# Kernel optimization log

Hardware: AMD Instinct MI355X
Metric: run time of the kernel (lower is better)

Reference implementation:

```python
import jax, jax.numpy as jnp
import numpy as np

N_NODES = 100000
N_EDGES = 3200000
N_GRAPHS = 4096
IN_DIM = 128
HID = 64
EPS = 1e-5


def setup_inputs() -> dict:
    key = jax.random.key(0)
    ks = jax.random.split(key, 16)
    x = jax.random.normal(ks[0], (N_NODES, IN_DIM), dtype=jnp.float32)
    edge_index = jax.random.randint(ks[1], (2, N_EDGES), 0, N_NODES, dtype=jnp.int32)
    batch = jnp.sort(jax.random.randint(ks[2], (N_NODES,), 0, N_GRAPHS, dtype=jnp.int32))

    def lin(k, fan_in, fan_out):
        s = 1.0 / np.sqrt(fan_in)
        kw, kb = jax.random.split(k)
        W = jax.random.uniform(kw, (fan_in, fan_out), minval=-s, maxval=s, dtype=jnp.float32)
        b = jax.random.uniform(kb, (fan_out,), minval=-s, maxval=s, dtype=jnp.float32)
        return W, b

    Wc0, bc0 = lin(ks[3], IN_DIM, HID)
    Wc1, bc1 = lin(ks[4], HID, HID)
    Wc2, bc2 = lin(ks[5], HID, HID)
    W1, b1 = lin(ks[6], HID, HID)
    W2, b2 = lin(ks[7], HID, 1)
    ones = jnp.ones((HID,), jnp.float32)
    zeros = jnp.zeros((HID,), jnp.float32)
    return {
        'x': x, 'edge_index': edge_index, 'batch': batch,
        'Wc0': Wc0, 'bc0': bc0, 'g0': ones, 'be0': zeros,
        'Wc1': Wc1, 'bc1': bc1, 'g1': ones, 'be1': zeros,
        'Wc2': Wc2, 'bc2': bc2, 'g2': ones, 'be2': zeros,
        'W1': W1, 'b1': b1, 'gf': ones, 'bf': zeros,
        'W2': W2, 'b2': b2,
    }


def _gcn_norm(edge_index):
    # Add self-loops, then symmetric normalization norm_e = d^-1/2[row] * d^-1/2[col]
    loops = jnp.arange(N_NODES, dtype=jnp.int32)
    row = jnp.concatenate([edge_index[0], loops])
    col = jnp.concatenate([edge_index[1], loops])
    deg = jax.ops.segment_sum(jnp.ones_like(col, jnp.float32), col, num_segments=N_NODES)
    dinv = jnp.where(deg > 0, jax.lax.rsqrt(deg), 0.0)
    norm = dinv[row] * dinv[col]
    return row, col, norm


def _gcn_conv(x, W, b, row, col, norm):
    h = x @ W                                   # [N, hid]
    msg = h[row] * norm[:, None]                # [E+N, hid] gather + scale
    out = jax.ops.segment_sum(msg, col, num_segments=N_NODES)  # scatter-add
    return out + b


def _bn(x, gamma, beta):
    mu = jnp.mean(x, axis=0)
    var = jnp.var(x, axis=0)
    return (x - mu) * jax.lax.rsqrt(var + EPS) * gamma + beta


def reference(x, edge_index, batch, Wc0, bc0, g0, be0, Wc1, bc1, g1, be1,
              Wc2, bc2, g2, be2, W1, b1, gf, bf, W2, b2):
    row, col, norm = _gcn_norm(edge_index)
    h = x
    for W, b, g, be in ((Wc0, bc0, g0, be0), (Wc1, bc1, g1, be1), (Wc2, bc2, g2, be2)):
        h = jax.nn.relu(_bn(_gcn_conv(h, W, b, row, col, norm), g, be))
    # global mean pool over graphs
    sums = jax.ops.segment_sum(h, batch, num_segments=N_GRAPHS)
    cnts = jax.ops.segment_sum(jnp.ones((N_NODES,), jnp.float32), batch, num_segments=N_GRAPHS)
    pooled = sums / jnp.maximum(cnts, 1.0)[:, None]  # [G, hid]
    z = jax.nn.relu(_bn(pooled @ W1 + b1, gf, bf))
    # dropout is identity at inference
    out = z @ W2 + b2
    return out.squeeze(-1)
```

## Files before the change

kernel.cpp:

```cpp
#include <hip/hip_runtime.h>
#include <hip/hip_bf16.h>

#define NN 100000
#define NE 3200000
#define NG 4096
#define NB 128
#define NBK 782

typedef unsigned short ushort_t;

__device__ __forceinline__ float bf2f(unsigned short u){
  union{unsigned int i; float f;} x; x.i = ((unsigned)u)<<16; return x.f;
}
__device__ __forceinline__ ushort_t f2bf(float f){
  union{float f; unsigned int i;} x; x.f = f;
  unsigned int r = x.i + 0x7fff + ((x.i >> 16) & 1);
  return (ushort_t)(r >> 16);
}


__global__ __launch_bounds__(256) void k_hist(const int* __restrict__ ei, int* __restrict__ histT){
  __shared__ int lh[NBK];
  int b = blockIdx.x, t = threadIdx.x;
  for (int k=t; k<NBK; k+=256) lh[k]=0;
  __syncthreads();
  int e0 = b*(NE/NB);
  for (int e=e0+t; e<e0+(NE/NB); e+=256) atomicAdd(&lh[ei[NE+e]>>7], 1);
  __syncthreads();
  for (int k=t; k<NBK; k+=256) histT[k*NB+b] = lh[k];
}

__global__ __launch_bounds__(256) void k_scanA(int* __restrict__ histT, int* __restrict__ total){
  int wv = blockIdx.x*4 + (threadIdx.x>>6);
  int lane = threadIdx.x & 63;
  if (wv >= NBK) return;
  int* row = histT + wv*NB;
  int a0 = row[lane], a1 = row[64+lane];
  int i0 = a0, i1 = a1;
  for (int off=1; off<64; off<<=1){
    int x = __shfl_up(i0, off, 64);
    int y = __shfl_up(i1, off, 64);
    if (lane >= off){ i0 += x; i1 += y; }
  }
  i1 += __shfl(i0, 63, 64);
  row[lane]    = i0 - a0;
  row[64+lane] = i1 - a1;
  if (lane==63) total[wv] = i1;
}

__global__ void k_scanB(const int* __restrict__ total, int* __restrict__ base){
  __shared__ int lds[1024];
  int t = threadIdx.x;
  int v = (t < NBK)? total[t] : 0;
  lds[t] = v; __syncthreads();
  for (int off=1; off<1024; off<<=1){
    int x = (t>=off)? lds[t-off] : 0;
    __syncthreads();
    lds[t] += x;
    __syncthreads();
  }
  if (t < NBK)      base[t]   = lds[t]-v;
  if (t == NBK-1)   base[NBK] = lds[t];
}

__global__ __launch_bounds__(256) void k_pairs(const int* __restrict__ ei,
    const int* __restrict__ histT, const int* __restrict__ base,
    int* __restrict__ pairs){
  __shared__ int cur[NBK];
  int b = blockIdx.x, t = threadIdx.x;
  for (int k=t; k<NBK; k+=256) cur[k] = base[k] + histT[k*NB + b];
  __syncthreads();
  int e0 = b*(NE/NB);
  for (int e=e0+t; e<e0+(NE/NB); e+=256){
    int src = ei[e], dst = ei[NE+e];
    int p = atomicAdd(&cur[dst>>7], 1);
    pairs[p] = (src << 7) | (dst & 127);
  }
}

__global__ __launch_bounds__(256) void k_fine(const int* __restrict__ pairs,
    const int* __restrict__ base, int* __restrict__ csr,
    int* __restrict__ colptr, float* __restrict__ dinv){
  __shared__ int cnt[128], off[128];
  int k = blockIdx.x, t = threadIdx.x;
  if (t < 128) cnt[t] = 0;
  __syncthreads();
  int s = base[k], e = base[k+1];
  for (int i=s+t; i<e; i+=256) atomicAdd(&cnt[pairs[i] & 127], 1);
  __syncthreads();
  int v = (t<128)? cnt[t] : 0;
  if (t<128) off[t] = v;
  __syncthreads();
  for (int o=1; o<128; o<<=1){
    int x = (t>=o && t<128)? off[t-o] : 0;
    __syncthreads();
    if (t<128) off[t] += x;
    __syncthreads();
  }
  int node0 = k*128;
  if (t < 128 && node0+t < NN){
    colptr[node0+t] = s + off[t] - v;
    dinv[node0+t]   = rsqrtf((float)cnt[t] + 1.0f);
  }
  if (k == NBK-1 && t == 0) colptr[NN] = NE;
  __syncthreads();
  if (t < 128) cnt[t] = off[t] - v;
  __syncthreads();
  for (int i=s+t; i<e; i+=256){
    int u = pairs[i];
    int p = s + atomicAdd(&cnt[u & 127], 1);
    csr[p] = u >> 7;
  }
}


template<int K>
__global__ __launch_bounds__(256) void k_gemm(const float* __restrict__ in_,
    const float* __restrict__ W, const float* __restrict__ dinv,
    ushort_t* __restrict__ out){
  __shared__ float Wl[K*64];
  int t = threadIdx.x;
  for (int i=t; i<K*64; i+=256) Wl[i] = W[i];
  __syncthreads();
  int c  = t & 63;
  int vb = __builtin_amdgcn_readfirstlane((int)(blockIdx.x*16 + (t>>6)*4));
  float acc0=0.f, acc1=0.f, acc2=0.f, acc3=0.f;
  const float4* x0 = (const float4*)(in_ + (size_t)vb*K);
  constexpr int RS = K/4;
  #pragma unroll 4
  for (int k4=0;k4<K/4;++k4){
    float4 a0 = x0[k4], a1 = x0[k4+RS], a2 = x0[k4+2*RS], a3 = x0[k4+3*RS];
    const float* wr = &Wl[k4*4*64 + c];
    float w0=wr[0], w1=wr[64], w2=wr[128], w3=wr[192];
    acc0 = fmaf(a0.x,w0,fmaf(a0.y,w1,fmaf(a0.z,w2,fmaf(a0.w,w3,acc0))));
    acc1 = fmaf(a1.x,w0,fmaf(a1.y,w1,fmaf(a1.z,w2,fmaf(a1.w,w3,acc1))));
    acc2 = fmaf(a2.x,w0,fmaf(a2.y,w1,fmaf(a2.z,w2,fmaf(a2.w,w3,acc2))));
    acc3 = fmaf(a3.x,w0,fmaf(a3.y,w1,fmaf(a3.z,w2,fmaf(a3.w,w3,acc3))));
  }
  float d0=dinv[vb], d1=dinv[vb+1], d2=dinv[vb+2], d3=dinv[vb+3];
  out[(size_t)(vb+0)*64+c]=f2bf(acc0*d0);
  out[(size_t)(vb+1)*64+c]=f2bf(acc1*d1);
  out[(size_t)(vb+2)*64+c]=f2bf(acc2*d2);
  out[(size_t)(vb+3)*64+c]=f2bf(acc3*d3);
}


__global__ __launch_bounds__(256) void k_aggregate(const ushort_t* __restrict__ hs,
    const int* __restrict__ colptr, const int* __restrict__ csr,
    const float* __restrict__ dinv, const float* __restrict__ bias,
    float* __restrict__ out, float* __restrict__ stats){
  int t = threadIdx.x; int c = t & 63;
  int wv = blockIdx.x*4 + (t>>6);
  float bc = bias[c];
  float s1 = 0.f, s2 = 0.f;
  for (int v = wv; v < NN; v += 8192){
    int vv = __builtin_amdgcn_readfirstlane(v);
    int e0 = colptr[vv], e1 = colptr[vv+1];
    float acc = bf2f(hs[(size_t)vv*64 + c]);
    int e = e0;
    for (; e+4 <= e1; e += 4){
      int i0=csr[e], i1=csr[e+1], i2=csr[e+2], i3=csr[e+3];
      float f0=bf2f(hs[(size_t)i0*64+c]), f1=bf2f(hs[(size_t)i1*64+c]);
      float f2=bf2f(hs[(size_t)i2*64+c]), f3=bf2f(hs[(size_t)i3*64+c]);
      acc += (f0+f1)+(f2+f3);
    }
    for (; e<e1; ++e) acc += bf2f(hs[(size_t)csr[e]*64+c]);
    float o = acc*dinv[vv] + bc;
    out[(size_t)vv*64+c] = o;
    s1 += o; s2 += o*o;
  }
  __shared__ float l1[256], l2[256];
  l1[t]=s1; l2[t]=s2; __syncthreads();
  if (t < 64){
    float a1 = l1[t]+l1[t+64]+l1[t+128]+l1[t+192];
    float a2 = l2[t]+l2[t+64]+l2[t+128]+l2[t+192];
    float* rep = stats + (size_t)(blockIdx.x & 31)*128;
    atomicAdd(&rep[t],    a1);
    atomicAdd(&rep[64+t], a2);
  }
}


__global__ void k_bncoeff(const float* __restrict__ stats, const float* __restrict__ g,
                          const float* __restrict__ be, float cnt, float* __restrict__ coeff){
  int c = threadIdx.x;
  float s1=0.f, s2=0.f;
  for (int r=0;r<32;++r){ s1 += stats[r*128+c]; s2 += stats[r*128+64+c]; }
  float mu  = s1/cnt;
  float var = s2/cnt - mu*mu;
  float a   = g[c]*rsqrtf(var + 1e-5f);
  coeff[c]    = a;
  coeff[64+c] = be[c] - mu*a;
}

__global__ __launch_bounds__(256) void k_bnapply(float* __restrict__ buf, const float* __restrict__ cf){
  int i = blockIdx.x*256 + threadIdx.x;
  float4 v = ((float4*)buf)[i];
  int c0 = (i & 15)*4;
  float a0=cf[c0+0], a1=cf[c0+1], a2=cf[c0+2], a3=cf[c0+3];
  float d0=cf[64+c0+0], d1=cf[64+c0+1], d2=cf[64+c0+2], d3=cf[64+c0+3];
  v.x = fmaxf(fmaf(v.x,a0,d0),0.f);
  v.y = fmaxf(fmaf(v.y,a1,d1),0.f);
  v.z = fmaxf(fmaf(v.z,a2,d2),0.f);
  v.w = fmaxf(fmaf(v.w,a3,d3),0.f);
  ((float4*)buf)[i] = v;
}


__global__ __launch_bounds__(256) void k_gbounds(const int* __restrict__ batch, int* __restrict__ gstart){
  int g = blockIdx.x*256 + threadIdx.x;
  int lo=0, hi=NN;
  while (lo<hi){ int mid=(lo+hi)>>1; if (batch[mid]<g) lo=mid+1; else hi=mid; }
  gstart[g]=lo;
  if (g==0) gstart[NG]=NN;
}

__global__ __launch_bounds__(256) void k_pool(const float* __restrict__ h, const int* __restrict__ gstart,
                                              float* __restrict__ pooled){
  int t=threadIdx.x; int c=t&63;
  int g = __builtin_amdgcn_readfirstlane((int)(blockIdx.x*4 + (t>>6)));
  int s = gstart[g], e = gstart[g+1];
  float acc=0.f;
  for (int v=s; v<e; ++v) acc += h[(size_t)v*64+c];
  float inv = 1.0f / fmaxf((float)(e-s), 1.0f);
  pooled[(size_t)g*64+c] = acc*inv;
}

__global__ __launch_bounds__(256) void k_tkern(float* __restrict__ pooled, const float* __restrict__ W1,
                                               const float* __restrict__ b1, float* __restrict__ stats){
  int t=threadIdx.x; int c=t&63;
  int g = __builtin_amdgcn_readfirstlane((int)(blockIdx.x*4 + (t>>6)));
  const float* p = pooled + (size_t)g*64;
  float acc = b1[c];
  #pragma unroll 4
  for (int k=0;k<64;++k) acc = fmaf(p[k], W1[k*64+c], acc);
  pooled[(size_t)g*64+c] = acc;
  float* rep = stats + (size_t)(blockIdx.x & 31)*128;
  atomicAdd(&rep[c],    acc);
  atomicAdd(&rep[64+c], acc*acc);
}

__global__ __launch_bounds__(256) void k_final(const float* __restrict__ tbuf, const float* __restrict__ gcf,
                                               const float* __restrict__ W2, const float* __restrict__ b2,
                                               float* __restrict__ out){
  int t=threadIdx.x; int c=t&63;
  int g = blockIdx.x*4 + (t>>6);
  float tv = tbuf[(size_t)g*64+c];
  float z  = fmaxf(fmaf(tv, gcf[c], gcf[64+c]), 0.f);
  float p  = z * W2[c];
  #pragma unroll
  for (int o=32;o>0;o>>=1) p += __shfl_xor(p, o, 64);
  if (c==0) out[g] = p + b2[0];
}


extern "C" void kernel_launch(void* const* d_in, const int* in_sizes, int n_in,
                              void* d_out, int out_size, void* d_ws, size_t ws_size,
                              hipStream_t stream) {
  const float* x    = (const float*)d_in[0];
  const int*   ei   = (const int*)d_in[1];
  const int*   batch= (const int*)d_in[2];
  const float* Wc0=(const float*)d_in[3],  *bc0=(const float*)d_in[4];
  const float* g0 =(const float*)d_in[5],  *be0=(const float*)d_in[6];
  const float* Wc1=(const float*)d_in[7],  *bc1=(const float*)d_in[8];
  const float* g1 =(const float*)d_in[9],  *be1=(const float*)d_in[10];
  const float* Wc2=(const float*)d_in[11], *bc2=(const float*)d_in[12];
  const float* g2 =(const float*)d_in[13], *be2=(const float*)d_in[14];
  const float* W1 =(const float*)d_in[15], *b1 =(const float*)d_in[16];
  const float* gf =(const float*)d_in[17], *bf_=(const float*)d_in[18];
  const float* W2 =(const float*)d_in[19], *b2 =(const float*)d_in[20];
  float* out = (float*)d_out;

  char* w = (char*)d_ws;
  float*    stats  = (float*)   (w + 0);
  int*      histT  = (int*)     (w + 65536);
  int*      total  = (int*)     (w + 465920);
  int*      base   = (int*)     (w + 469056);
  int*      colptr = (int*)     (w + 472192);
  float*    dinv   = (float*)   (w + 872208);
  int*      gstart = (int*)     (w + 1272208);
  float*    coeff  = (float*)   (w + 1288608);
  float*    gcoeff = (float*)   (w + 1289120);
  float*    pooled = (float*)   (w + 1289632);
  int*      csr    = (int*)     (w + 2338240);
  ushort_t* bufA   = (ushort_t*)(w + 15138240);
  float*    bufB   = (float*)   (w + 27938240);
  int*      pairs  = (int*)bufB;

  hipMemsetAsync(stats, 0, 65536, stream);

  k_hist <<<NB,  256,  0, stream>>>(ei, histT);
  k_scanA<<<196, 256,  0, stream>>>(histT, total);
  k_scanB<<<1,   1024, 0, stream>>>(total, base);
  k_pairs<<<NB,  256,  0, stream>>>(ei, histT, base, pairs);
  k_fine <<<NBK, 256,  0, stream>>>(pairs, base, csr, colptr, dinv);

  k_gemm<128><<<NN/16, 256, 0, stream>>>(x, Wc0, dinv, bufA);
  k_aggregate<<<2048, 256, 0, stream>>>(bufA, colptr, csr, dinv, bc0, bufB, stats + 0*4096);
  k_bncoeff<<<1, 64, 0, stream>>>(stats + 0*4096, g0, be0, (float)NN, coeff);
  k_bnapply<<<NN*16/256, 256, 0, stream>>>(bufB, coeff);
  k_gemm<64><<<NN/16, 256, 0, stream>>>(bufB, Wc1, dinv, bufA);
  k_aggregate<<<2048, 256, 0, stream>>>(bufA, colptr, csr, dinv, bc1, bufB, stats + 1*4096);
  k_bncoeff<<<1, 64, 0, stream>>>(stats + 1*4096, g1, be1, (float)NN, coeff);
  k_bnapply<<<NN*16/256, 256, 0, stream>>>(bufB, coeff);
  k_gemm<64><<<NN/16, 256, 0, stream>>>(bufB, Wc2, dinv, bufA);
  k_aggregate<<<2048, 256, 0, stream>>>(bufA, colptr, csr, dinv, bc2, bufB, stats + 2*4096);
  k_bncoeff<<<1, 64, 0, stream>>>(stats + 2*4096, g2, be2, (float)NN, coeff);
  k_bnapply<<<NN*16/256, 256, 0, stream>>>(bufB, coeff);

  k_gbounds<<<NG/256, 256, 0, stream>>>(batch, gstart);
  k_pool   <<<NG/4,   256, 0, stream>>>(bufB, gstart, pooled);
  k_tkern  <<<NG/4,   256, 0, stream>>>(pooled, W1, b1, stats + 3*4096);
  k_bncoeff<<<1, 64, 0, stream>>>(stats + 3*4096, gf, bf_, (float)NG, gcoeff);
  k_final  <<<NG/4,   256, 0, stream>>>(pooled, gcoeff, W2, b2, out);
}
```

Measured before the change: 674.2 us.

## Split feature matrices into 16-column strips and aggregate one strip per pass

The bf16 node features and the fp32 layer outputs are stored as four 16-column strips instead of one 64-wide row. Aggregation now runs four passes, each gathering only one strip, so the gathered working set per pass (about 3.2 MB) is more likely to stay in cache, at the cost of reading the CSR indices four times and making four times as many launches. The GEMM, bnapply and pool kernels are adapted to the strip layout. The CSR build also doubles its block count and block size, and histT now reuses the csr buffer's space.

```diff
diff --git a/kernel.cpp b/kernel.cpp
--- a/kernel.cpp
+++ b/kernel.cpp
@@ -4,8 +4,9 @@
 #define NN 100000
 #define NE 3200000
 #define NG 4096
-#define NB 128
+#define NB 256
 #define NBK 782
+#define NST 4
 
 typedef unsigned short ushort_t;
 
@@ -19,33 +20,35 @@
 }
 
 
-__global__ __launch_bounds__(256) void k_hist(const int* __restrict__ ei, int* __restrict__ histT){
+__global__ __launch_bounds__(512) void k_hist(const int* __restrict__ ei, int* __restrict__ histT){
   __shared__ int lh[NBK];
   int b = blockIdx.x, t = threadIdx.x;
-  for (int k=t; k<NBK; k+=256) lh[k]=0;
+  for (int k=t; k<NBK; k+=512) lh[k]=0;
   __syncthreads();
   int e0 = b*(NE/NB);
-  for (int e=e0+t; e<e0+(NE/NB); e+=256) atomicAdd(&lh[ei[NE+e]>>7], 1);
-  __syncthreads();
-  for (int k=t; k<NBK; k+=256) histT[k*NB+b] = lh[k];
+  for (int e=e0+t; e<e0+(NE/NB); e+=512) atomicAdd(&lh[ei[NE+e]>>7], 1);
+  __syncthreads();
+  for (int k=t; k<NBK; k+=512) histT[(size_t)k*NB+b] = lh[k];
 }
 
 __global__ __launch_bounds__(256) void k_scanA(int* __restrict__ histT, int* __restrict__ total){
   int wv = blockIdx.x*4 + (threadIdx.x>>6);
   int lane = threadIdx.x & 63;
   if (wv >= NBK) return;
-  int* row = histT + wv*NB;
-  int a0 = row[lane], a1 = row[64+lane];
-  int i0 = a0, i1 = a1;
-  for (int off=1; off<64; off<<=1){
-    int x = __shfl_up(i0, off, 64);
-    int y = __shfl_up(i1, off, 64);
-    if (lane >= off){ i0 += x; i1 += y; }
-  }
-  i1 += __shfl(i0, 63, 64);
-  row[lane]    = i0 - a0;
-  row[64+lane] = i1 - a1;
-  if (lane==63) total[wv] = i1;
+  int* row = histT + (size_t)wv*NB;
+  int carry = 0;
+  #pragma unroll
+  for (int ch=0; ch<NB/64; ++ch){
+    int a = row[ch*64+lane];
+    int inc = a;
+    for (int off=1; off<64; off<<=1){
+      int x = __shfl_up(inc, off, 64);
+      if (lane >= off) inc += x;
+    }
+    row[ch*64+lane] = carry + inc - a;
+    carry += __shfl(inc, 63, 64);
+  }
+  if (lane==0) total[wv] = carry;
 }
 
 __global__ void k_scanB(const int* __restrict__ total, int* __restrict__ base){
@@ -63,15 +66,15 @@
   if (t == NBK-1)   base[NBK] = lds[t];
 }
 
-__global__ __launch_bounds__(256) void k_pairs(const int* __restrict__ ei,
+__global__ __launch_bounds__(512) void k_pairs(const int* __restrict__ ei,
     const int* __restrict__ histT, const int* __restrict__ base,
     int* __restrict__ pairs){
   __shared__ int cur[NBK];
   int b = blockIdx.x, t = threadIdx.x;
-  for (int k=t; k<NBK; k+=256) cur[k] = base[k] + histT[k*NB + b];
+  for (int k=t; k<NBK; k+=512) cur[k] = base[k] + histT[(size_t)k*NB + b];
   __syncthreads();
   int e0 = b*(NE/NB);
-  for (int e=e0+t; e<e0+(NE/NB); e+=256){
+  for (int e=e0+t; e<e0+(NE/NB); e+=512){
     int src = ei[e], dst = ei[NE+e];
     int p = atomicAdd(&cur[dst>>7], 1);
     pairs[p] = (src << 7) | (dst & 127);
@@ -114,22 +117,20 @@
 }
 
 
-template<int K>
-__global__ __launch_bounds__(256) void k_gemm(const float* __restrict__ in_,
+__global__ __launch_bounds__(256) void k_gemm0(const float* __restrict__ in_,
     const float* __restrict__ W, const float* __restrict__ dinv,
     ushort_t* __restrict__ out){
-  __shared__ float Wl[K*64];
+  __shared__ float Wl[128*64];
   int t = threadIdx.x;
-  for (int i=t; i<K*64; i+=256) Wl[i] = W[i];
+  for (int i=t; i<128*64; i+=256) Wl[i] = W[i];
   __syncthreads();
   int c  = t & 63;
   int vb = __builtin_amdgcn_readfirstlane((int)(blockIdx.x*16 + (t>>6)*4));
   float acc0=0.f, acc1=0.f, acc2=0.f, acc3=0.f;
-  const float4* x0 = (const float4*)(in_ + (size_t)vb*K);
-  constexpr int RS = K/4;
+  const float4* x0 = (const float4*)(in_ + (size_t)vb*128);
   #pragma unroll 4
-  for (int k4=0;k4<K/4;++k4){
-    float4 a0 = x0[k4], a1 = x0[k4+RS], a2 = x0[k4+2*RS], a3 = x0[k4+3*RS];
+  for (int k4=0;k4<32;++k4){
+    float4 a0 = x0[k4], a1 = x0[k4+32], a2 = x0[k4+64], a3 = x0[k4+96];
     const float* wr = &Wl[k4*4*64 + c];
     float w0=wr[0], w1=wr[64], w2=wr[128], w3=wr[192];
     acc0 = fmaf(a0.x,w0,fmaf(a0.y,w1,fmaf(a0.z,w2,fmaf(a0.w,w3,acc0))));
@@ -138,45 +139,83 @@
     acc3 = fmaf(a3.x,w0,fmaf(a3.y,w1,fmaf(a3.z,w2,fmaf(a3.w,w3,acc3))));
   }
   float d0=dinv[vb], d1=dinv[vb+1], d2=dinv[vb+2], d3=dinv[vb+3];
-  out[(size_t)(vb+0)*64+c]=f2bf(acc0*d0);
-  out[(size_t)(vb+1)*64+c]=f2bf(acc1*d1);
-  out[(size_t)(vb+2)*64+c]=f2bf(acc2*d2);
-  out[(size_t)(vb+3)*64+c]=f2bf(acc3*d3);
-}
-
-
-__global__ __launch_bounds__(256) void k_aggregate(const ushort_t* __restrict__ hs,
+  size_t sb = (size_t)(c>>4)*NN*16 + (c&15);
+  out[sb + (size_t)(vb+0)*16]=f2bf(acc0*d0);
+  out[sb + (size_t)(vb+1)*16]=f2bf(acc1*d1);
+  out[sb + (size_t)(vb+2)*16]=f2bf(acc2*d2);
+  out[sb + (size_t)(vb+3)*16]=f2bf(acc3*d3);
+}
+
+
+__global__ __launch_bounds__(256) void k_gemmS(const float* __restrict__ in_,
+    const float* __restrict__ W, const float* __restrict__ dinv,
+    ushort_t* __restrict__ out){
+  __shared__ float Wl[64*64];
+  int t = threadIdx.x;
+  for (int i=t; i<64*64; i+=256) Wl[i] = W[i];
+  __syncthreads();
+  int c  = t & 63;
+  int vb = __builtin_amdgcn_readfirstlane((int)(blockIdx.x*16 + (t>>6)*4));
+  float acc0=0.f, acc1=0.f, acc2=0.f, acc3=0.f;
+  #pragma unroll
+  for (int s=0;s<4;++s){
+    const float4* xs0 = (const float4*)(in_ + ((size_t)s*NN + vb+0)*16);
+    const float4* xs1 = (const float4*)(in_ + ((size_t)s*NN + vb+1)*16);
+    const float4* xs2 = (const float4*)(in_ + ((size_t)s*NN + vb+2)*16);
+    const float4* xs3 = (const float4*)(in_ + ((size_t)s*NN + vb+3)*16);
+    #pragma unroll
+    for (int j=0;j<4;++j){
+      float4 a0 = xs0[j], a1 = xs1[j], a2 = xs2[j], a3 = xs3[j];
+      const float* wr = &Wl[(s*16 + j*4)*64 + c];
+      float w0=wr[0], w1=wr[64], w2=wr[128], w3=wr[192];
+      acc0 = fmaf(a0.x,w0,fmaf(a0.y,w1,fmaf(a0.z,w2,fmaf(a0.w,w3,acc0))));
+      acc1 = fmaf(a1.x,w0,fmaf(a1.y,w1,fmaf(a1.z,w2,fmaf(a1.w,w3,acc1))));
+      acc2 = fmaf(a2.x,w0,fmaf(a2.y,w1,fmaf(a2.z,w2,fmaf(a2.w,w3,acc2))));
+      acc3 = fmaf(a3.x,w0,fmaf(a3.y,w1,fmaf(a3.z,w2,fmaf(a3.w,w3,acc3))));
+    }
+  }
+  float d0=dinv[vb], d1=dinv[vb+1], d2=dinv[vb+2], d3=dinv[vb+3];
+  size_t sb = (size_t)(c>>4)*NN*16 + (c&15);
+  out[sb + (size_t)(vb+0)*16]=f2bf(acc0*d0);
+  out[sb + (size_t)(vb+1)*16]=f2bf(acc1*d1);
+  out[sb + (size_t)(vb+2)*16]=f2bf(acc2*d2);
+  out[sb + (size_t)(vb+3)*16]=f2bf(acc3*d3);
+}
+
+
+__global__ __launch_bounds__(256) void k_aggstrip(const ushort_t* __restrict__ hsS,
     const int* __restrict__ colptr, const int* __restrict__ csr,
     const float* __restrict__ dinv, const float* __restrict__ bias,
-    float* __restrict__ out, float* __restrict__ stats){
-  int t = threadIdx.x; int c = t & 63;
-  int wv = blockIdx.x*4 + (t>>6);
-  float bc = bias[c];
-  float s1 = 0.f, s2 = 0.f;
-  for (int v = wv; v < NN; v += 8192){
-    int vv = __builtin_amdgcn_readfirstlane(v);
-    int e0 = colptr[vv], e1 = colptr[vv+1];
-    float acc = bf2f(hs[(size_t)vv*64 + c]);
-    int e = e0;
-    for (; e+4 <= e1; e += 4){
-      int i0=csr[e], i1=csr[e+1], i2=csr[e+2], i3=csr[e+3];
-      float f0=bf2f(hs[(size_t)i0*64+c]), f1=bf2f(hs[(size_t)i1*64+c]);
-      float f2=bf2f(hs[(size_t)i2*64+c]), f3=bf2f(hs[(size_t)i3*64+c]);
-      acc += (f0+f1)+(f2+f3);
-    }
-    for (; e<e1; ++e) acc += bf2f(hs[(size_t)csr[e]*64+c]);
-    float o = acc*dinv[vv] + bc;
-    out[(size_t)vv*64+c] = o;
-    s1 += o; s2 += o*o;
-  }
+    float* __restrict__ outS, float* __restrict__ stats, int s){
+  int t = threadIdx.x;
+  int cc = t & 15;
+  int grp = t >> 4;
+  int vv = blockIdx.x*16 + grp;
+  const ushort_t* strip = hsS + (size_t)s*NN*16;
+  int e0 = colptr[vv], e1 = colptr[vv+1];
+  float acc = bf2f(strip[(size_t)vv*16+cc]);
+  int e = e0;
+  for (; e < e1 && (e & 3); ++e) acc += bf2f(strip[(size_t)csr[e]*16+cc]);
+  for (; e+4 <= e1; e += 4){
+    int4 q = *(const int4*)(csr + e);
+    float f0 = bf2f(strip[(size_t)q.x*16+cc]);
+    float f1 = bf2f(strip[(size_t)q.y*16+cc]);
+    float f2 = bf2f(strip[(size_t)q.z*16+cc]);
+    float f3 = bf2f(strip[(size_t)q.w*16+cc]);
+    acc += (f0+f1)+(f2+f3);
+  }
+  for (; e<e1; ++e) acc += bf2f(strip[(size_t)csr[e]*16+cc]);
+  float o = acc*dinv[vv] + bias[s*16+cc];
+  outS[((size_t)s*NN + vv)*16 + cc] = o;
   __shared__ float l1[256], l2[256];
-  l1[t]=s1; l2[t]=s2; __syncthreads();
-  if (t < 64){
-    float a1 = l1[t]+l1[t+64]+l1[t+128]+l1[t+192];
-    float a2 = l2[t]+l2[t+64]+l2[t+128]+l2[t+192];
+  l1[t]=o; l2[t]=o*o; __syncthreads();
+  if (t < 16){
+    float a1=0.f, a2=0.f;
+    #pragma unroll
+    for (int g=0; g<16; ++g){ a1 += l1[g*16+t]; a2 += l2[g*16+t]; }
     float* rep = stats + (size_t)(blockIdx.x & 31)*128;
-    atomicAdd(&rep[t],    a1);
-    atomicAdd(&rep[64+t], a2);
+    atomicAdd(&rep[s*16+t],      a1);
+    atomicAdd(&rep[64+s*16+t],   a2);
   }
 }
 
@@ -195,8 +234,9 @@
 
 __global__ __launch_bounds__(256) void k_bnapply(float* __restrict__ buf, const float* __restrict__ cf){
   int i = blockIdx.x*256 + threadIdx.x;
-  float4 v = ((float4*)buf)[i];
-  int c0 = (i & 15)*4;
+  float4 v = ((const float4*)buf)[i];
+  int s  = i / (NN*4);
+  int c0 = s*16 + (i & 3)*4;
   float a0=cf[c0+0], a1=cf[c0+1], a2=cf[c0+2], a3=cf[c0+3];
   float d0=cf[64+c0+0], d1=cf[64+c0+1], d2=cf[64+c0+2], d3=cf[64+c0+3];
   v.x = fmaxf(fmaf(v.x,a0,d0),0.f);
@@ -220,8 +260,9 @@
   int t=threadIdx.x; int c=t&63;
   int g = __builtin_amdgcn_readfirstlane((int)(blockIdx.x*4 + (t>>6)));
   int s = gstart[g], e = gstart[g+1];
+  const float* hp = h + (size_t)(c>>4)*NN*16 + (c&15);
   float acc=0.f;
-  for (int v=s; v<e; ++v) acc += h[(size_t)v*64+c];
+  for (int v=s; v<e; ++v) acc += hp[(size_t)v*16];
   float inv = 1.0f / fmaxf((float)(e-s), 1.0f);
   pooled[(size_t)g*64+c] = acc*inv;
 }
@@ -273,38 +314,41 @@
 
   char* w = (char*)d_ws;
   float*    stats  = (float*)   (w + 0);
-  int*      histT  = (int*)     (w + 65536);
-  int*      total  = (int*)     (w + 465920);
-  int*      base   = (int*)     (w + 469056);
-  int*      colptr = (int*)     (w + 472192);
-  float*    dinv   = (float*)   (w + 872208);
-  int*      gstart = (int*)     (w + 1272208);
-  float*    coeff  = (float*)   (w + 1288608);
-  float*    gcoeff = (float*)   (w + 1289120);
-  float*    pooled = (float*)   (w + 1289632);
-  int*      csr    = (int*)     (w + 2338240);
-  ushort_t* bufA   = (ushort_t*)(w + 15138240);
-  float*    bufB   = (float*)   (w + 27938240);
+  int*      total  = (int*)     (w + 65536);
+  int*      base   = (int*)     (w + 68736);
+  int*      colptr = (int*)     (w + 71936);
+  float*    dinv   = (float*)   (w + 471952);
+  int*      gstart = (int*)     (w + 871952);
+  float*    coeff  = (float*)   (w + 888352);
+  float*    gcoeff = (float*)   (w + 888864);
+  float*    pooled = (float*)   (w + 889392);
+  int*      csr    = (int*)     (w + 1937968);
+  ushort_t* bufA   = (ushort_t*)(w + 14737968);
+  float*    bufB   = (float*)   (w + 27537968);
+  int*      histT  = csr;
   int*      pairs  = (int*)bufB;
 
   hipMemsetAsync(stats, 0, 65536, stream);
 
-  k_hist <<<NB,  256,  0, stream>>>(ei, histT);
+  k_hist <<<NB,  512,  0, stream>>>(ei, histT);
   k_scanA<<<196, 256,  0, stream>>>(histT, total);
   k_scanB<<<1,   1024, 0, stream>>>(total, base);
-  k_pairs<<<NB,  256,  0, stream>>>(ei, histT, base, pairs);
+  k_pairs<<<NB,  512,  0, stream>>>(ei, histT, base, pairs);
   k_fine <<<NBK, 256,  0, stream>>>(pairs, base, csr, colptr, dinv);
 
-  k_gemm<128><<<NN/16, 256, 0, stream>>>(x, Wc0, dinv, bufA);
-  k_aggregate<<<2048, 256, 0, stream>>>(bufA, colptr, csr, dinv, bc0, bufB, stats + 0*4096);
+  k_gemm0<<<NN/16, 256, 0, stream>>>(x, Wc0, dinv, bufA);
+  for (int s=0;s<NST;++s)
+    k_aggstrip<<<NN/16, 256, 0, stream>>>(bufA, colptr, csr, dinv, bc0, bufB, stats + 0*4096, s);
   k_bncoeff<<<1, 64, 0, stream>>>(stats + 0*4096, g0, be0, (float)NN, coeff);
   k_bnapply<<<NN*16/256, 256, 0, stream>>>(bufB, coeff);
-  k_gemm<64><<<NN/16, 256, 0, stream>>>(bufB, Wc1, dinv, bufA);
-  k_aggregate<<<2048, 256, 0, stream>>>(bufA, colptr, csr, dinv, bc1, bufB, stats + 1*4096);
+  k_gemmS<<<NN/16, 256, 0, stream>>>(bufB, Wc1, dinv, bufA);
+  for (int s=0;s<NST;++s)
+    k_aggstrip<<<NN/16, 256, 0, stream>>>(bufA, colptr, csr, dinv, bc1, bufB, stats + 1*4096, s);
   k_bncoeff<<<1, 64, 0, stream>>>(stats + 1*4096, g1, be1, (float)NN, coeff);
   k_bnapply<<<NN*16/256, 256, 0, stream>>>(bufB, coeff);
-  k_gemm<64><<<NN/16, 256, 0, stream>>>(bufB, Wc2, dinv, bufA);
-  k_aggregate<<<2048, 256, 0, stream>>>(bufA, colptr, csr, dinv, bc2, bufB, stats + 2*4096);
+  k_gemmS<<<NN/16, 256, 0, stream>>>(bufB, Wc2, dinv, bufA);
+  for (int s=0;s<NST;++s)
+    k_aggstrip<<<NN/16, 256, 0, stream>>>(bufA, colptr, csr, dinv, bc2, bufB, stats + 2*4096, s);
   k_bncoeff<<<1, 64, 0, stream>>>(stats + 2*4096, g2, be2, (float)NN, coeff);
   k_bnapply<<<NN*16/256, 256, 0, stream>>>(bufB, coeff);
 
```

Result: slower. 856.2 us (+27.0%).

## Partition CSR neighbors by source range and aggregate in phased source-range passes

Applied to the files above, without the earlier changes.

The CSR build now sorts each destination's neighbors into four source-index ranges and records per-range sub-pointers. The aggregation kernel keeps 25 node accumulators per thread and processes one source range at a time across all its nodes, with a block barrier between phases. The goal is to confine gathers from the bf16 feature buffer to a quarter-sized working set so they hit in cache more often. The histogram and pair kernels also move to 256 blocks of 512 threads, and workspace buffers are reordered and aliased. In exchange it adds register pressure, a larger sub-pointer array and barrier stalls, and less parallelism per node.

```diff
diff --git a/kernel.cpp b/kernel.cpp
--- a/kernel.cpp
+++ b/kernel.cpp
@@ -4,8 +4,9 @@
 #define NN 100000
 #define NE 3200000
 #define NG 4096
-#define NB 128
+#define NB 256
 #define NBK 782
+#define RSZ 25000
 
 typedef unsigned short ushort_t;
 
@@ -17,35 +18,40 @@
   unsigned int r = x.i + 0x7fff + ((x.i >> 16) & 1);
   return (ushort_t)(r >> 16);
 }
-
-
-__global__ __launch_bounds__(256) void k_hist(const int* __restrict__ ei, int* __restrict__ histT){
+__device__ __forceinline__ int src_rng(int s){
+  return (s>=RSZ) + (s>=2*RSZ) + (s>=3*RSZ);
+}
+
+
+__global__ __launch_bounds__(512) void k_hist(const int* __restrict__ ei, int* __restrict__ histT){
   __shared__ int lh[NBK];
   int b = blockIdx.x, t = threadIdx.x;
-  for (int k=t; k<NBK; k+=256) lh[k]=0;
+  for (int k=t; k<NBK; k+=512) lh[k]=0;
   __syncthreads();
   int e0 = b*(NE/NB);
-  for (int e=e0+t; e<e0+(NE/NB); e+=256) atomicAdd(&lh[ei[NE+e]>>7], 1);
-  __syncthreads();
-  for (int k=t; k<NBK; k+=256) histT[k*NB+b] = lh[k];
+  for (int e=e0+t; e<e0+(NE/NB); e+=512) atomicAdd(&lh[ei[NE+e]>>7], 1);
+  __syncthreads();
+  for (int k=t; k<NBK; k+=512) histT[(size_t)k*NB+b] = lh[k];
 }
 
 __global__ __launch_bounds__(256) void k_scanA(int* __restrict__ histT, int* __restrict__ total){
   int wv = blockIdx.x*4 + (threadIdx.x>>6);
   int lane = threadIdx.x & 63;
   if (wv >= NBK) return;
-  int* row = histT + wv*NB;
-  int a0 = row[lane], a1 = row[64+lane];
-  int i0 = a0, i1 = a1;
-  for (int off=1; off<64; off<<=1){
-    int x = __shfl_up(i0, off, 64);
-    int y = __shfl_up(i1, off, 64);
-    if (lane >= off){ i0 += x; i1 += y; }
-  }
-  i1 += __shfl(i0, 63, 64);
-  row[lane]    = i0 - a0;
-  row[64+lane] = i1 - a1;
-  if (lane==63) total[wv] = i1;
+  int* row = histT + (size_t)wv*NB;
+  int carry = 0;
+  #pragma unroll
+  for (int ch=0; ch<NB/64; ++ch){
+    int a = row[ch*64+lane];
+    int inc = a;
+    for (int off=1; off<64; off<<=1){
+      int x = __shfl_up(inc, off, 64);
+      if (lane >= off) inc += x;
+    }
+    row[ch*64+lane] = carry + inc - a;
+    carry += __shfl(inc, 63, 64);
+  }
+  if (lane==0) total[wv] = carry;
 }
 
 __global__ void k_scanB(const int* __restrict__ total, int* __restrict__ base){
@@ -63,15 +69,15 @@
   if (t == NBK-1)   base[NBK] = lds[t];
 }
 
-__global__ __launch_bounds__(256) void k_pairs(const int* __restrict__ ei,
+__global__ __launch_bounds__(512) void k_pairs(const int* __restrict__ ei,
     const int* __restrict__ histT, const int* __restrict__ base,
     int* __restrict__ pairs){
   __shared__ int cur[NBK];
   int b = blockIdx.x, t = threadIdx.x;
-  for (int k=t; k<NBK; k+=256) cur[k] = base[k] + histT[k*NB + b];
+  for (int k=t; k<NBK; k+=512) cur[k] = base[k] + histT[(size_t)k*NB + b];
   __syncthreads();
   int e0 = b*(NE/NB);
-  for (int e=e0+t; e<e0+(NE/NB); e+=256){
+  for (int e=e0+t; e<e0+(NE/NB); e+=512){
     int src = ei[e], dst = ei[NE+e];
     int p = atomicAdd(&cur[dst>>7], 1);
     pairs[p] = (src << 7) | (dst & 127);
@@ -80,36 +86,50 @@
 
 __global__ __launch_bounds__(256) void k_fine(const int* __restrict__ pairs,
     const int* __restrict__ base, int* __restrict__ csr,
-    int* __restrict__ colptr, float* __restrict__ dinv){
-  __shared__ int cnt[128], off[128];
+    int* __restrict__ colptr, int* __restrict__ subp, float* __restrict__ dinv){
+  __shared__ int cnt[512], off[512], ps[256];
   int k = blockIdx.x, t = threadIdx.x;
-  if (t < 128) cnt[t] = 0;
+  cnt[t]=0; cnt[t+256]=0;
   __syncthreads();
   int s = base[k], e = base[k+1];
-  for (int i=s+t; i<e; i+=256) atomicAdd(&cnt[pairs[i] & 127], 1);
-  __syncthreads();
-  int v = (t<128)? cnt[t] : 0;
-  if (t<128) off[t] = v;
-  __syncthreads();
-  for (int o=1; o<128; o<<=1){
-    int x = (t>=o && t<128)? off[t-o] : 0;
-    __syncthreads();
-    if (t<128) off[t] += x;
-    __syncthreads();
-  }
+  for (int i=s+t; i<e; i+=256){
+    int u = pairs[i];
+    atomicAdd(&cnt[((u&127)<<2) | src_rng(u>>7)], 1);
+  }
+  __syncthreads();
+  int a = cnt[2*t], b = cnt[2*t+1];
+  int p = a+b;
+  ps[t]=p; __syncthreads();
+  for (int o=1;o<256;o<<=1){
+    int x=(t>=o)? ps[t-o]:0;
+    __syncthreads();
+    ps[t]+=x;
+    __syncthreads();
+  }
+  int excl = ps[t]-p;
+  off[2*t]=excl; off[2*t+1]=excl+a;
+  __syncthreads();
   int node0 = k*128;
   if (t < 128 && node0+t < NN){
-    colptr[node0+t] = s + off[t] - v;
-    dinv[node0+t]   = rsqrtf((float)cnt[t] + 1.0f);
+    int d4 = t<<2;
+    colptr[node0+t] = s + off[d4];
+    int deg = cnt[d4]+cnt[d4+1]+cnt[d4+2]+cnt[d4+3];
+    dinv[node0+t]   = rsqrtf((float)deg + 1.0f);
+    subp[(node0+t)*4+0] = s + off[d4+0];
+    subp[(node0+t)*4+1] = s + off[d4+1];
+    subp[(node0+t)*4+2] = s + off[d4+2];
+    subp[(node0+t)*4+3] = s + off[d4+3];
   }
   if (k == NBK-1 && t == 0) colptr[NN] = NE;
   __syncthreads();
-  if (t < 128) cnt[t] = off[t] - v;
+  cnt[t]=off[t]; cnt[t+256]=off[t+256];
   __syncthreads();
   for (int i=s+t; i<e; i+=256){
     int u = pairs[i];
-    int p = s + atomicAdd(&cnt[u & 127], 1);
-    csr[p] = u >> 7;
+    int src = u>>7;
+    int key = ((u&127)<<2) | src_rng(src);
+    int pp = s + atomicAdd(&cnt[key], 1);
+    csr[pp] = src;
   }
 }
 
@@ -145,29 +165,53 @@
 }
 
 
-__global__ __launch_bounds__(256) void k_aggregate(const ushort_t* __restrict__ hs,
-    const int* __restrict__ colptr, const int* __restrict__ csr,
-    const float* __restrict__ dinv, const float* __restrict__ bias,
-    float* __restrict__ out, float* __restrict__ stats){
-  int t = threadIdx.x; int c = t & 63;
+#define AGG_W 4096
+#define AGG_V 25
+
+__global__ __launch_bounds__(256,4) void k_aggP(const ushort_t* __restrict__ hs,
+    const int* __restrict__ colptr, const int* __restrict__ subp,
+    const int* __restrict__ csr, const float* __restrict__ dinv,
+    const float* __restrict__ bias, float* __restrict__ out,
+    float* __restrict__ stats){
+  int t = threadIdx.x, c = t & 63;
   int wv = blockIdx.x*4 + (t>>6);
+  float acc[AGG_V];
+  #pragma unroll
+  for (int i=0;i<AGG_V;++i){
+    int v = wv + i*AGG_W;
+    acc[i] = (v<NN)? bf2f(hs[(size_t)v*64+c]) : 0.f;
+  }
+  for (int r=0;r<4;++r){
+    #pragma unroll
+    for (int i=0;i<AGG_V;++i){
+      int v = wv + i*AGG_W;
+      if (v < NN){
+        int e0 = subp[v*4+r];
+        int e1 = (r<3)? subp[v*4+r+1] : colptr[v+1];
+        float a = acc[i];
+        int e = e0;
+        for (; e+4<=e1; e+=4){
+          int i0=csr[e], i1=csr[e+1], i2=csr[e+2], i3=csr[e+3];
+          float f0=bf2f(hs[(size_t)i0*64+c]), f1=bf2f(hs[(size_t)i1*64+c]);
+          float f2=bf2f(hs[(size_t)i2*64+c]), f3=bf2f(hs[(size_t)i3*64+c]);
+          a += (f0+f1)+(f2+f3);
+        }
+        for (; e<e1; ++e) a += bf2f(hs[(size_t)csr[e]*64+c]);
+        acc[i] = a;
+      }
+    }
+    __syncthreads();
+  }
   float bc = bias[c];
-  float s1 = 0.f, s2 = 0.f;
-  for (int v = wv; v < NN; v += 8192){
-    int vv = __builtin_amdgcn_readfirstlane(v);
-    int e0 = colptr[vv], e1 = colptr[vv+1];
-    float acc = bf2f(hs[(size_t)vv*64 + c]);
-    int e = e0;
-    for (; e+4 <= e1; e += 4){
-      int i0=csr[e], i1=csr[e+1], i2=csr[e+2], i3=csr[e+3];
-      float f0=bf2f(hs[(size_t)i0*64+c]), f1=bf2f(hs[(size_t)i1*64+c]);
-      float f2=bf2f(hs[(size_t)i2*64+c]), f3=bf2f(hs[(size_t)i3*64+c]);
-      acc += (f0+f1)+(f2+f3);
+  float s1=0.f, s2=0.f;
+  #pragma unroll
+  for (int i=0;i<AGG_V;++i){
+    int v = wv + i*AGG_W;
+    if (v < NN){
+      float o = acc[i]*dinv[v] + bc;
+      out[(size_t)v*64+c] = o;
+      s1 += o; s2 += o*o;
     }
-    for (; e<e1; ++e) acc += bf2f(hs[(size_t)csr[e]*64+c]);
-    float o = acc*dinv[vv] + bc;
-    out[(size_t)vv*64+c] = o;
-    s1 += o; s2 += o*o;
   }
   __shared__ float l1[256], l2[256];
   l1[t]=s1; l2[t]=s2; __syncthreads();
@@ -195,7 +239,7 @@
 
 __global__ __launch_bounds__(256) void k_bnapply(float* __restrict__ buf, const float* __restrict__ cf){
   int i = blockIdx.x*256 + threadIdx.x;
-  float4 v = ((float4*)buf)[i];
+  float4 v = ((const float4*)buf)[i];
   int c0 = (i & 15)*4;
   float a0=cf[c0+0], a1=cf[c0+1], a2=cf[c0+2], a3=cf[c0+3];
   float d0=cf[64+c0+0], d1=cf[64+c0+1], d2=cf[64+c0+2], d3=cf[64+c0+3];
@@ -273,38 +317,39 @@
 
   char* w = (char*)d_ws;
   float*    stats  = (float*)   (w + 0);
-  int*      histT  = (int*)     (w + 65536);
-  int*      total  = (int*)     (w + 465920);
-  int*      base   = (int*)     (w + 469056);
-  int*      colptr = (int*)     (w + 472192);
-  float*    dinv   = (float*)   (w + 872208);
-  int*      gstart = (int*)     (w + 1272208);
-  float*    coeff  = (float*)   (w + 1288608);
-  float*    gcoeff = (float*)   (w + 1289120);
-  float*    pooled = (float*)   (w + 1289632);
-  int*      csr    = (int*)     (w + 2338240);
-  ushort_t* bufA   = (ushort_t*)(w + 15138240);
-  float*    bufB   = (float*)   (w + 27938240);
+  int*      total  = (int*)     (w + 65536);
+  int*      base   = (int*)     (w + 68736);
+  int*      colptr = (int*)     (w + 71936);
+  int*      subp   = (int*)     (w + 471952);
+  float*    dinv   = (float*)   (w + 2071952);
+  int*      gstart = (int*)     (w + 2471952);
+  float*    coeff  = (float*)   (w + 2488352);
+  float*    gcoeff = (float*)   (w + 2488864);
+  int*      csr    = (int*)     (w + 2489392);
+  ushort_t* bufA   = (ushort_t*)(w + 15289392);
+  float*    bufB   = (float*)   (w + 28089392);
+  int*      histT  = csr;
   int*      pairs  = (int*)bufB;
+  float*    pooled = (float*)subp;
 
   hipMemsetAsync(stats, 0, 65536, stream);
 
-  k_hist <<<NB,  256,  0, stream>>>(ei, histT);
+  k_hist <<<NB,  512,  0, stream>>>(ei, histT);
   k_scanA<<<196, 256,  0, stream>>>(histT, total);
   k_scanB<<<1,   1024, 0, stream>>>(total, base);
-  k_pairs<<<NB,  256,  0, stream>>>(ei, histT, base, pairs);
-  k_fine <<<NBK, 256,  0, stream>>>(pairs, base, csr, colptr, dinv);
+  k_pairs<<<NB,  512,  0, stream>>>(ei, histT, base, pairs);
+  k_fine <<<NBK, 256,  0, stream>>>(pairs, base, csr, colptr, subp, dinv);
 
   k_gemm<128><<<NN/16, 256, 0, stream>>>(x, Wc0, dinv, bufA);
-  k_aggregate<<<2048, 256, 0, stream>>>(bufA, colptr, csr, dinv, bc0, bufB, stats + 0*4096);
+  k_aggP<<<1024, 256, 0, stream>>>(bufA, colptr, subp, csr, dinv, bc0, bufB, stats + 0*4096);
   k_bncoeff<<<1, 64, 0, stream>>>(stats + 0*4096, g0, be0, (float)NN, coeff);
   k_bnapply<<<NN*16/256, 256, 0, stream>>>(bufB, coeff);
   k_gemm<64><<<NN/16, 256, 0, stream>>>(bufB, Wc1, dinv, bufA);
-  k_aggregate<<<2048, 256, 0, stream>>>(bufA, colptr, csr, dinv, bc1, bufB, stats + 1*4096);
+  k_aggP<<<1024, 256, 0, stream>>>(bufA, colptr, subp, csr, dinv, bc1, bufB, stats + 1*4096);
   k_bncoeff<<<1, 64, 0, stream>>>(stats + 1*4096, g1, be1, (float)NN, coeff);
   k_bnapply<<<NN*16/256, 256, 0, stream>>>(bufB, coeff);
   k_gemm<64><<<NN/16, 256, 0, stream>>>(bufB, Wc2, dinv, bufA);
-  k_aggregate<<<2048, 256, 0, stream>>>(bufA, colptr, csr, dinv, bc2, bufB, stats + 2*4096);
+  k_aggP<<<1024, 256, 0, stream>>>(bufA, colptr, subp, csr, dinv, bc2, bufB, stats + 2*4096);
   k_bncoeff<<<1, 64, 0, stream>>>(stats + 2*4096, g2, be2, (float)NN, coeff);
   k_bnapply<<<NN*16/256, 256, 0, stream>>>(bufB, coeff);
 
```

Result: slower. 1.153 ms (+71.0%).

## Fuse BN-apply into MFMA bf16 GEMMs and pooling; widen CSR build blocks

Applied to the files above, without the earlier changes.

Replaces the scalar FMA GEMMs with bf16 MFMA 16x16x32 kernels, converting inputs and weights to bf16 on the fly. It removes the separate BN+ReLU apply passes by folding the normalization into the next GEMM's operand load and into the pooling loop. It also doubles the number of blocks and threads used for the histogram and pair-bucketing stages, and reuses the CSR buffer for the histogram. The aim is to cut three full read-write passes over the activation buffer and to speed up the dense projections. The cost is lower GEMM input precision from bf16 rounding of x and W.

```diff
diff --git a/kernel.cpp b/kernel.cpp
--- a/kernel.cpp
+++ b/kernel.cpp
@@ -4,10 +4,12 @@
 #define NN 100000
 #define NE 3200000
 #define NG 4096
-#define NB 128
+#define NB 256
 #define NBK 782
 
 typedef unsigned short ushort_t;
+typedef short short8 __attribute__((ext_vector_type(8)));
+typedef float floatx4 __attribute__((ext_vector_type(4)));
 
 __device__ __forceinline__ float bf2f(unsigned short u){
   union{unsigned int i; float f;} x; x.i = ((unsigned)u)<<16; return x.f;
@@ -19,33 +21,35 @@
 }
 
 
-__global__ __launch_bounds__(256) void k_hist(const int* __restrict__ ei, int* __restrict__ histT){
+__global__ __launch_bounds__(512) void k_hist(const int* __restrict__ ei, int* __restrict__ histT){
   __shared__ int lh[NBK];
   int b = blockIdx.x, t = threadIdx.x;
-  for (int k=t; k<NBK; k+=256) lh[k]=0;
+  for (int k=t; k<NBK; k+=512) lh[k]=0;
   __syncthreads();
   int e0 = b*(NE/NB);
-  for (int e=e0+t; e<e0+(NE/NB); e+=256) atomicAdd(&lh[ei[NE+e]>>7], 1);
-  __syncthreads();
-  for (int k=t; k<NBK; k+=256) histT[k*NB+b] = lh[k];
+  for (int e=e0+t; e<e0+(NE/NB); e+=512) atomicAdd(&lh[ei[NE+e]>>7], 1);
+  __syncthreads();
+  for (int k=t; k<NBK; k+=512) histT[(size_t)k*NB+b] = lh[k];
 }
 
 __global__ __launch_bounds__(256) void k_scanA(int* __restrict__ histT, int* __restrict__ total){
   int wv = blockIdx.x*4 + (threadIdx.x>>6);
   int lane = threadIdx.x & 63;
   if (wv >= NBK) return;
-  int* row = histT + wv*NB;
-  int a0 = row[lane], a1 = row[64+lane];
-  int i0 = a0, i1 = a1;
-  for (int off=1; off<64; off<<=1){
-    int x = __shfl_up(i0, off, 64);
-    int y = __shfl_up(i1, off, 64);
-    if (lane >= off){ i0 += x; i1 += y; }
-  }
-  i1 += __shfl(i0, 63, 64);
-  row[lane]    = i0 - a0;
-  row[64+lane] = i1 - a1;
-  if (lane==63) total[wv] = i1;
+  int* row = histT + (size_t)wv*NB;
+  int carry = 0;
+  #pragma unroll
+  for (int ch=0; ch<NB/64; ++ch){
+    int a = row[ch*64+lane];
+    int inc = a;
+    for (int off=1; off<64; off<<=1){
+      int x = __shfl_up(inc, off, 64);
+      if (lane >= off) inc += x;
+    }
+    row[ch*64+lane] = carry + inc - a;
+    carry += __shfl(inc, 63, 64);
+  }
+  if (lane==0) total[wv] = carry;
 }
 
 __global__ void k_scanB(const int* __restrict__ total, int* __restrict__ base){
@@ -63,15 +67,15 @@
   if (t == NBK-1)   base[NBK] = lds[t];
 }
 
-__global__ __launch_bounds__(256) void k_pairs(const int* __restrict__ ei,
+__global__ __launch_bounds__(512) void k_pairs(const int* __restrict__ ei,
     const int* __restrict__ histT, const int* __restrict__ base,
     int* __restrict__ pairs){
   __shared__ int cur[NBK];
   int b = blockIdx.x, t = threadIdx.x;
-  for (int k=t; k<NBK; k+=256) cur[k] = base[k] + histT[k*NB + b];
+  for (int k=t; k<NBK; k+=512) cur[k] = base[k] + histT[(size_t)k*NB + b];
   __syncthreads();
   int e0 = b*(NE/NB);
-  for (int e=e0+t; e<e0+(NE/NB); e+=256){
+  for (int e=e0+t; e<e0+(NE/NB); e+=512){
     int src = ei[e], dst = ei[NE+e];
     int p = atomicAdd(&cur[dst>>7], 1);
     pairs[p] = (src << 7) | (dst & 127);
@@ -114,34 +118,100 @@
 }
 
 
-template<int K>
-__global__ __launch_bounds__(256) void k_gemm(const float* __restrict__ in_,
+__global__ __launch_bounds__(256) void k_gemm0m(const float* __restrict__ x,
     const float* __restrict__ W, const float* __restrict__ dinv,
-    ushort_t* __restrict__ out){
-  __shared__ float Wl[K*64];
+    ushort_t* __restrict__ hs){
+  __shared__ __attribute__((aligned(16))) ushort_t Wt[64*136];
   int t = threadIdx.x;
-  for (int i=t; i<K*64; i+=256) Wl[i] = W[i];
-  __syncthreads();
-  int c  = t & 63;
-  int vb = __builtin_amdgcn_readfirstlane((int)(blockIdx.x*16 + (t>>6)*4));
-  float acc0=0.f, acc1=0.f, acc2=0.f, acc3=0.f;
-  const float4* x0 = (const float4*)(in_ + (size_t)vb*K);
-  constexpr int RS = K/4;
-  #pragma unroll 4
-  for (int k4=0;k4<K/4;++k4){
-    float4 a0 = x0[k4], a1 = x0[k4+RS], a2 = x0[k4+2*RS], a3 = x0[k4+3*RS];
-    const float* wr = &Wl[k4*4*64 + c];
-    float w0=wr[0], w1=wr[64], w2=wr[128], w3=wr[192];
-    acc0 = fmaf(a0.x,w0,fmaf(a0.y,w1,fmaf(a0.z,w2,fmaf(a0.w,w3,acc0))));
-    acc1 = fmaf(a1.x,w0,fmaf(a1.y,w1,fmaf(a1.z,w2,fmaf(a1.w,w3,acc1))));
-    acc2 = fmaf(a2.x,w0,fmaf(a2.y,w1,fmaf(a2.z,w2,fmaf(a2.w,w3,acc2))));
-    acc3 = fmaf(a3.x,w0,fmaf(a3.y,w1,fmaf(a3.z,w2,fmaf(a3.w,w3,acc3))));
-  }
-  float d0=dinv[vb], d1=dinv[vb+1], d2=dinv[vb+2], d3=dinv[vb+3];
-  out[(size_t)(vb+0)*64+c]=f2bf(acc0*d0);
-  out[(size_t)(vb+1)*64+c]=f2bf(acc1*d1);
-  out[(size_t)(vb+2)*64+c]=f2bf(acc2*d2);
-  out[(size_t)(vb+3)*64+c]=f2bf(acc3*d3);
+  for (int i=t; i<128*64; i+=256){
+    int k = i>>6, n = i&63;
+    Wt[n*136 + k] = f2bf(W[i]);
+  }
+  __syncthreads();
+  int lane = t & 63, wv = t >> 6;
+  int n0 = lane & 15, quad = lane >> 4;
+  int r0 = blockIdx.x*64 + wv*16;
+  int row = r0 + n0;
+  int rowc = (row < NN)? row : NN-1;
+  const float* xr = x + (size_t)rowc*128 + quad*8;
+  floatx4 acc[4] = {{0,0,0,0},{0,0,0,0},{0,0,0,0},{0,0,0,0}};
+  #pragma unroll
+  for (int ks=0; ks<4; ++ks){
+    float4 a01 = *(const float4*)(xr + ks*32);
+    float4 a23 = *(const float4*)(xr + ks*32 + 4);
+    short8 af;
+    af[0]=(short)f2bf(a01.x); af[1]=(short)f2bf(a01.y);
+    af[2]=(short)f2bf(a01.z); af[3]=(short)f2bf(a01.w);
+    af[4]=(short)f2bf(a23.x); af[5]=(short)f2bf(a23.y);
+    af[6]=(short)f2bf(a23.z); af[7]=(short)f2bf(a23.w);
+    #pragma unroll
+    for (int tl=0; tl<4; ++tl){
+      short8 bf = *(const short8*)(&Wt[(tl*16+n0)*136 + ks*32 + quad*8]);
+      acc[tl] = __builtin_amdgcn_mfma_f32_16x16x32_bf16(af, bf, acc[tl], 0, 0, 0);
+    }
+  }
+  #pragma unroll
+  for (int reg=0; reg<4; ++reg){
+    int rr = r0 + quad*4 + reg;
+    if (rr < NN){
+      float dv = dinv[rr];
+      #pragma unroll
+      for (int tl=0; tl<4; ++tl)
+        hs[(size_t)rr*64 + tl*16 + n0] = f2bf(acc[tl][reg]*dv);
+    }
+  }
+}
+
+
+__global__ __launch_bounds__(256) void k_gemmSm(const float* __restrict__ h,
+    const float* __restrict__ W, const float* __restrict__ coeff,
+    const float* __restrict__ dinv, ushort_t* __restrict__ hs){
+  __shared__ __attribute__((aligned(16))) ushort_t Wt[64*72];
+  int t = threadIdx.x;
+  for (int i=t; i<64*64; i+=256){
+    int k = i>>6, n = i&63;
+    Wt[n*72 + k] = f2bf(W[i]);
+  }
+  __syncthreads();
+  int lane = t & 63, wv = t >> 6;
+  int n0 = lane & 15, quad = lane >> 4;
+  int r0 = blockIdx.x*64 + wv*16;
+  int row = r0 + n0;
+  int rowc = (row < NN)? row : NN-1;
+  const float* hr = h + (size_t)rowc*64 + quad*8;
+  floatx4 acc[4] = {{0,0,0,0},{0,0,0,0},{0,0,0,0},{0,0,0,0}};
+  #pragma unroll
+  for (int ks=0; ks<2; ++ks){
+    float4 a01 = *(const float4*)(hr + ks*32);
+    float4 a23 = *(const float4*)(hr + ks*32 + 4);
+    const float* cA = coeff + ks*32 + quad*8;
+    float4 ca0 = *(const float4*)(cA),      ca1 = *(const float4*)(cA+4);
+    float4 cb0 = *(const float4*)(cA+64),   cb1 = *(const float4*)(cA+68);
+    short8 af;
+    af[0]=(short)f2bf(fmaxf(fmaf(a01.x,ca0.x,cb0.x),0.f));
+    af[1]=(short)f2bf(fmaxf(fmaf(a01.y,ca0.y,cb0.y),0.f));
+    af[2]=(short)f2bf(fmaxf(fmaf(a01.z,ca0.z,cb0.z),0.f));
+    af[3]=(short)f2bf(fmaxf(fmaf(a01.w,ca0.w,cb0.w),0.f));
+    af[4]=(short)f2bf(fmaxf(fmaf(a23.x,ca1.x,cb1.x),0.f));
+    af[5]=(short)f2bf(fmaxf(fmaf(a23.y,ca1.y,cb1.y),0.f));
+    af[6]=(short)f2bf(fmaxf(fmaf(a23.z,ca1.z,cb1.z),0.f));
+    af[7]=(short)f2bf(fmaxf(fmaf(a23.w,ca1.w,cb1.w),0.f));
+    #pragma unroll
+    for (int tl=0; tl<4; ++tl){
+      short8 bf = *(const short8*)(&Wt[(tl*16+n0)*72 + ks*32 + quad*8]);
+      acc[tl] = __builtin_amdgcn_mfma_f32_16x16x32_bf16(af, bf, acc[tl], 0, 0, 0);
+    }
+  }
+  #pragma unroll
+  for (int reg=0; reg<4; ++reg){
+    int rr = r0 + quad*4 + reg;
+    if (rr < NN){
+      float dv = dinv[rr];
+      #pragma unroll
+      for (int tl=0; tl<4; ++tl)
+        hs[(size_t)rr*64 + tl*16 + n0] = f2bf(acc[tl][reg]*dv);
+    }
+  }
 }
 
 
@@ -193,19 +263,6 @@
   coeff[64+c] = be[c] - mu*a;
 }
 
-__global__ __launch_bounds__(256) void k_bnapply(float* __restrict__ buf, const float* __restrict__ cf){
-  int i = blockIdx.x*256 + threadIdx.x;
-  float4 v = ((float4*)buf)[i];
-  int c0 = (i & 15)*4;
-  float a0=cf[c0+0], a1=cf[c0+1], a2=cf[c0+2], a3=cf[c0+3];
-  float d0=cf[64+c0+0], d1=cf[64+c0+1], d2=cf[64+c0+2], d3=cf[64+c0+3];
-  v.x = fmaxf(fmaf(v.x,a0,d0),0.f);
-  v.y = fmaxf(fmaf(v.y,a1,d1),0.f);
-  v.z = fmaxf(fmaf(v.z,a2,d2),0.f);
-  v.w = fmaxf(fmaf(v.w,a3,d3),0.f);
-  ((float4*)buf)[i] = v;
-}
-
 
 __global__ __launch_bounds__(256) void k_gbounds(const int* __restrict__ batch, int* __restrict__ gstart){
   int g = blockIdx.x*256 + threadIdx.x;
@@ -216,12 +273,13 @@
 }
 
 __global__ __launch_bounds__(256) void k_pool(const float* __restrict__ h, const int* __restrict__ gstart,
-                                              float* __restrict__ pooled){
+                                              const float* __restrict__ cf, float* __restrict__ pooled){
   int t=threadIdx.x; int c=t&63;
   int g = __builtin_amdgcn_readfirstlane((int)(blockIdx.x*4 + (t>>6)));
   int s = gstart[g], e = gstart[g+1];
+  float a = cf[c], d = cf[64+c];
   float acc=0.f;
-  for (int v=s; v<e; ++v) acc += h[(size_t)v*64+c];
+  for (int v=s; v<e; ++v) acc += fmaxf(fmaf(h[(size_t)v*64+c], a, d), 0.f);
   float inv = 1.0f / fmaxf((float)(e-s), 1.0f);
   pooled[(size_t)g*64+c] = acc*inv;
 }
@@ -273,43 +331,40 @@
 
   char* w = (char*)d_ws;
   float*    stats  = (float*)   (w + 0);
-  int*      histT  = (int*)     (w + 65536);
-  int*      total  = (int*)     (w + 465920);
-  int*      base   = (int*)     (w + 469056);
-  int*      colptr = (int*)     (w + 472192);
-  float*    dinv   = (float*)   (w + 872208);
-  int*      gstart = (int*)     (w + 1272208);
-  float*    coeff  = (float*)   (w + 1288608);
-  float*    gcoeff = (float*)   (w + 1289120);
-  float*    pooled = (float*)   (w + 1289632);
-  int*      csr    = (int*)     (w + 2338240);
-  ushort_t* bufA   = (ushort_t*)(w + 15138240);
-  float*    bufB   = (float*)   (w + 27938240);
+  int*      total  = (int*)     (w + 65536);
+  int*      base   = (int*)     (w + 68736);
+  int*      colptr = (int*)     (w + 71936);
+  float*    dinv   = (float*)   (w + 471952);
+  int*      gstart = (int*)     (w + 871952);
+  float*    coeff  = (float*)   (w + 888352);
+  float*    gcoeff = (float*)   (w + 888864);
+  float*    pooled = (float*)   (w + 889376);
+  int*      csr    = (int*)     (w + 1937968);
+  ushort_t* bufA   = (ushort_t*)(w + 14737968);
+  float*    bufB   = (float*)   (w + 27537968);
+  int*      histT  = csr;
   int*      pairs  = (int*)bufB;
 
   hipMemsetAsync(stats, 0, 65536, stream);
 
-  k_hist <<<NB,  256,  0, stream>>>(ei, histT);
+  k_hist <<<NB,  512,  0, stream>>>(ei, histT);
   k_scanA<<<196, 256,  0, stream>>>(histT, total);
   k_scanB<<<1,   1024, 0, stream>>>(total, base);
-  k_pairs<<<NB,  256,  0, stream>>>(ei, histT, base, pairs);
+  k_pairs<<<NB,  512,  0, stream>>>(ei, histT, base, pairs);
   k_fine <<<NBK, 256,  0, stream>>>(pairs, base, csr, colptr, dinv);
 
-  k_gemm<128><<<NN/16, 256, 0, stream>>>(x, Wc0, dinv, bufA);
+  k_gemm0m<<<1563, 256, 0, stream>>>(x, Wc0, dinv, bufA);
   k_aggregate<<<2048, 256, 0, stream>>>(bufA, colptr, csr, dinv, bc0, bufB, stats + 0*4096);
   k_bncoeff<<<1, 64, 0, stream>>>(stats + 0*4096, g0, be0, (float)NN, coeff);
-  k_bnapply<<<NN*16/256, 256, 0, stream>>>(bufB, coeff);
-  k_gemm<64><<<NN/16, 256, 0, stream>>>(bufB, Wc1, dinv, bufA);
+  k_gemmSm<<<1563, 256, 0, stream>>>(bufB, Wc1, coeff, dinv, bufA);
   k_aggregate<<<2048, 256, 0, stream>>>(bufA, colptr, csr, dinv, bc1, bufB, stats + 1*4096);
   k_bncoeff<<<1, 64, 0, stream>>>(stats + 1*4096, g1, be1, (float)NN, coeff);
-  k_bnapply<<<NN*16/256, 256, 0, stream>>>(bufB, coeff);
-  k_gemm<64><<<NN/16, 256, 0, stream>>>(bufB, Wc2, dinv, bufA);
+  k_gemmSm<<<1563, 256, 0, stream>>>(bufB, Wc2, coeff, dinv, bufA);
   k_aggregate<<<2048, 256, 0, stream>>>(bufA, colptr, csr, dinv, bc2, bufB, stats + 2*4096);
   k_bncoeff<<<1, 64, 0, stream>>>(stats + 2*4096, g2, be2, (float)NN, coeff);
-  k_bnapply<<<NN*16/256, 256, 0, stream>>>(bufB, coeff);
 
   k_gbounds<<<NG/256, 256, 0, stream>>>(batch, gstart);
-  k_pool   <<<NG/4,   256, 0, stream>>>(bufB, gstart, pooled);
+  k_pool   <<<NG/4,   256, 0, stream>>>(bufB, gstart, coeff, pooled);
   k_tkern  <<<NG/4,   256, 0, stream>>>(pooled, W1, b1, stats + 3*4096);
   k_bncoeff<<<1, 64, 0, stream>>>(stats + 3*4096, gf, bf_, (float)NG, gcoeff);
   k_final  <<<NG/4,   256, 0, stream>>>(pooled, gcoeff, W2, b2, out);
```

Measured after the change: 557.3 us. -17.3%, faster.
